# Kernel optimization log

Measured on AMD Instinct MI355X. Metric: run time of the kernel, lower is better.

## Reference

```python
import jax, jax.numpy as jnp
import numpy as np
from jax import lax

DIM = 128; HEADS = 8; SPLIT = 4; MLP = 4
B = 8; H = 64; W = 64
EPS = 1e-5

def conv1x1(x, w, b):
    # x: (b,c,h,w), w: (o,c), b: (o,)
    return jnp.einsum('oc,bchw->bohw', w, x) + b[None, :, None, None]

def dwconv3(x, w, b):
    # depthwise 3x3, w: (C,1,3,3)
    c = x.shape[1]
    y = lax.conv_general_dilated(x, w, window_strides=(1, 1), padding=((1, 1), (1, 1)),
                                 feature_group_count=c,
                                 dimension_numbers=('NCHW', 'OIHW', 'NCHW'))
    return y + b[None, :, None, None]

def groupnorm1(x, g, bta):
    # GroupNorm with 1 group: normalize over (C,H,W) per sample
    mu = x.mean(axis=(1, 2, 3), keepdims=True)
    var = ((x - mu) ** 2).mean(axis=(1, 2, 3), keepdims=True)
    xn = (x - mu) * lax.rsqrt(var + EPS)
    return xn * g[None, :, None, None] + bta[None, :, None, None]

def eca(x, w):
    b, c, h, w_ = x.shape
    y = x.mean(axis=(2, 3))                         # (b,c)
    y = lax.conv_general_dilated(y[:, None, :], w, window_strides=(1,), padding=((2, 2),),
                                 dimension_numbers=('NCH', 'OIH', 'NCH'))  # (b,1,c)
    gate = jax.nn.sigmoid(y[:, 0])[:, :, None, None]
    return x * gate

def esa(x, alpha):
    x_se = x - x.mean(axis=(2, 3), keepdims=True)   # subtract per-channel GAP
    x_max = x_se.max(axis=1, keepdims=True)
    x_min = x_se.min(axis=1, keepdims=True)
    a = alpha[0]
    return x * jax.nn.sigmoid(x_max) * a + x * jax.nn.sigmoid(x_min) * (1.0 - a)

def eaa(q, k, v, h_sp, w_sp, cpe_w, cpe_b):
    b, c, h, w = q.shape
    hd = c // HEADS
    nh, nw = h // h_sp, w // w_sp
    L = h_sp * w_sp
    cpe = dwconv3(v, cpe_w, cpe_b)
    def win(t):
        t = t.reshape(b, c, nh, h_sp, nw, w_sp)
        t = t.transpose(0, 2, 4, 3, 5, 1).reshape(-1, L, HEADS, hd)
        return t.transpose(0, 2, 1, 3)  # (b*nh*nw, heads, L, hd)
    qw, kw, vw = win(q), win(k), win(v)
    attn = jax.nn.softmax(qw @ kw.transpose(0, 1, 3, 2), axis=-1)  # no scale, as in source
    o = attn @ vw                                    # (b*nh*nw, heads, L, hd)
    o = o.transpose(0, 2, 1, 3).reshape(b, nh, nw, h_sp, w_sp, c)
    o = o.transpose(0, 5, 1, 3, 2, 4).reshape(b, c, h, w)
    return o + cpe

def setup_inputs() -> dict:
    key = jax.random.key(0)
    ks = jax.random.split(key, 16)
    d = DIM
    z = lambda *s: jnp.zeros(s, jnp.float32)
    def n(i, shape, s=0.02):
        return jax.random.normal(ks[i], shape, dtype=jnp.float32) * s
    return dict(
        x=jax.random.normal(ks[0], (B, d, H, W), dtype=jnp.float32),
        eca_w=n(1, (1, 1, 5), 0.2),
        esa_alpha=jnp.ones((1,), jnp.float32),
        cpe1_w=n(2, (d, 1, 3, 3), 0.1), cpe1_b=z(d),
        g1=jnp.ones((d,), jnp.float32), b1=z(d),
        actp_w=n(3, (d, d)), actp_b=z(d),
        inp_w=n(4, (d, d)), inp_b=z(d),
        dwc_w=n(5, (d, 1, 3, 3), 0.1), dwc_b=z(d),
        qkv_w=n(6, (5 * d, d)), qkv_b=z(5 * d),
        eaax_w=n(7, (d, 1, 3, 3), 0.1), eaax_b=z(d),
        eaay_w=n(8, (d, 1, 3, 3), 0.1), eaay_b=z(d),
        outp_w=n(9, (d, d)), outp_b=z(d),
        cpe2_w=n(10, (d, 1, 3, 3), 0.1), cpe2_b=z(d),
        g2=jnp.ones((d,), jnp.float32), b2=z(d),
        mlp1_w=n(11, (MLP * d, d)), mlp1_b=z(MLP * d),
        mlp2_w=n(12, (d, MLP * d)), mlp2_b=z(d),
    )

def reference(x, eca_w, esa_alpha, cpe1_w, cpe1_b, g1, b1, actp_w, actp_b, inp_w, inp_b,
              dwc_w, dwc_b, qkv_w, qkv_b, eaax_w, eaax_b, eaay_w, eaay_b, outp_w, outp_b,
              cpe2_w, cpe2_b, g2, b2, mlp1_w, mlp1_b, mlp2_w, mlp2_b):
    b, c, h, w = x.shape
    x = eca(x, eca_w) + esa(x, esa_alpha)
    x = x + dwconv3(x, cpe1_w, cpe1_b)
    shortcut = x
    xn = groupnorm1(x, g1, b1)
    act_res = jax.nn.relu(conv1x1(xn, actp_w, actp_b))
    t = jax.nn.relu(dwconv3(conv1x1(xn, inp_w, inp_b), dwc_w, dwc_b))
    t = conv1x1(t, qkv_w, qkv_b)                     # (b, 5c, h, w)
    t5 = t.reshape(b, c, 5, h, w)                    # channel i::5 == t5[:,:,i]
    q0, k0, v0, q1, k1 = (t5[:, :, i] for i in range(5))
    a = eaa(q0, k0, v0, h, SPLIT, eaax_w, eaax_b) + eaa(q1, k1, v0, SPLIT, w, eaay_w, eaay_b)
    out = conv1x1(a * act_res, outp_w, outp_b) + shortcut
    out = out + dwconv3(out, cpe2_w, cpe2_b)
    mlp = conv1x1(jax.nn.relu(conv1x1(groupnorm1(out, g2, b2), mlp1_w, mlp1_b)), mlp2_w, mlp2_b)
    return mlp + out
```

## Files before the change

kernel.cpp:

```cpp
#include <hip/hip_runtime.h>

#define NPIX 4096
#define CDIM 128
#define BATCH 8
#define EPSN 1e-5f
#define LOG2E 1.44269504088896340736f

typedef __attribute__((ext_vector_type(8))) short short8;
typedef __attribute__((ext_vector_type(4))) float f32x4;
typedef __attribute__((ext_vector_type(16))) float f32x16;

__device__ __forceinline__ float sigmoidf_(float x) { return 1.f / (1.f + __expf(-x)); }

__device__ __forceinline__ unsigned short f2b(float f) {
    unsigned int u = __float_as_uint(f);
    unsigned int r = (u + 0x7FFF + ((u >> 16) & 1)) >> 16;
    return (unsigned short)r;
}
__device__ __forceinline__ float b2f(unsigned short u) {
    return __uint_as_float((unsigned int)u << 16);
}

__device__ __forceinline__ void pl32swap(unsigned int& a, unsigned int& b) {
    asm("v_permlane32_swap_b32 %0, %1" : "+v"(a), "+v"(b));
}

__device__ __forceinline__ int tok2pix(int mode, int wi, int l) {
    return (mode == 0) ? ((l >> 2) * 64 + wi * 4 + (l & 3))
                       : ((wi * 4 + (l >> 6)) * 64 + (l & 63));
}

__global__ __launch_bounds__(256) void convert_w_kernel(const float* __restrict__ qkv_w,
                                                        const float* __restrict__ mlp1_w,
                                                        const float* __restrict__ mlp2_w,
                                                        const float* __restrict__ actp_w,
                                                        const float* __restrict__ inp_w,
                                                        const float* __restrict__ outp_w,
                                                        const float* __restrict__ qkv_b,
                                                        const float* __restrict__ eaax_w,
                                                        const float* __restrict__ eaax_b,
                                                        const float* __restrict__ eaay_w,
                                                        const float* __restrict__ eaay_b,
                                                        const float* __restrict__ cpe1_w,
                                                        const float* __restrict__ dwc_w,
                                                        const float* __restrict__ cpe2_w,
                                                        const float* __restrict__ actp_b,
                                                        const float* __restrict__ inp_b,
                                                        unsigned short* __restrict__ dst,
                                                        float* __restrict__ qb_r,
                                                        float* __restrict__ wsT,
                                                        float* __restrict__ bsum,
                                                        float* __restrict__ cpe1T,
                                                        float* __restrict__ dwcT,
                                                        float* __restrict__ cpe2T,
                                                        float* __restrict__ abi,
                                                        float* __restrict__ gstats) {
    int i = blockIdx.x * 256 + threadIdx.x;
    if (i >= 267776) {
        if (i < 269824) gstats[i - 267776] = 0.f;
        return;
    }
    if (i < 262144) {
        float v;
        if (i < 81920) {
            int o = i >> 7, c = i & 127;
            int g = o >> 7;
            v = qkv_w[(size_t)(5 * (o & 127) + g) * 128 + c];
            if (g == 0 || g == 3) v *= LOG2E;
        } else if (i < 147456) v = mlp1_w[i - 81920];
        else if (i < 212992)   v = mlp2_w[i - 147456];
        else if (i < 229376)   v = actp_w[i - 212992];
        else if (i < 245760)   v = inp_w[i - 229376];
        else                   v = outp_w[i - 245760];
        dst[i] = f2b(v);
    } else {
        int j = i - 262144;
        if (j < 640) {
            int g = j >> 7;
            float v = qkv_b[5 * (j & 127) + g];
            if (g == 0 || g == 3) v *= LOG2E;
            qb_r[j] = v;
        }
        else if (j < 1792) {
            int idx = j - 640; int k = idx >> 7, c = idx & 127;
            wsT[idx] = eaax_w[c * 9 + k] + eaay_w[c * 9 + k];
        } else if (j < 1920) bsum[j - 1792] = eaax_b[j - 1792] + eaay_b[j - 1792];
        else if (j < 3072) {
            int idx = j - 1920; int k = idx >> 7, c = idx & 127;
            cpe1T[idx] = cpe1_w[c * 9 + k];
        } else if (j < 4224) {
            int idx = j - 3072; int k = idx >> 7, c = idx & 127;
            dwcT[idx] = dwc_w[c * 9 + k];
        } else if (j < 5376) {
            int idx = j - 4224; int k = idx >> 7, c = idx & 127;
            cpe2T[idx] = cpe2_w[c * 9 + k];
        } else {
            int idx = j - 5376;
            abi[idx] = (idx < 128) ? actp_b[idx] : inp_b[idx - 128];
        }
    }
}

__global__ __launch_bounds__(256) void mean_bc_kernel(const float* __restrict__ x,
                                                      float* __restrict__ mean) {
    __shared__ float sb[4];
    int bc = blockIdx.x;
    const float* p = x + (size_t)bc * NPIX;
    float s = 0.f;
    for (int i = threadIdx.x; i < NPIX; i += 256) s += p[i];
#pragma unroll
    for (int off = 32; off > 0; off >>= 1) s += __shfl_down(s, off, 64);
    if ((threadIdx.x & 63) == 0) sb[threadIdx.x >> 6] = s;
    __syncthreads();
    if (threadIdx.x == 0) mean[bc] = (sb[0] + sb[1] + sb[2] + sb[3]) * (1.f / (float)NPIX);
}

__global__ __launch_bounds__(256) void esa_tr_kernel(const float* __restrict__ x,
                                                     const float* __restrict__ mean,
                                                     const float* __restrict__ w5,
                                                     const float* __restrict__ alpha_p,
                                                     float* __restrict__ y) {
    __shared__ float tile[128][65];
    __shared__ float smx[4][64], smn[4][64], ssc[64], gat[128];
    int b = blockIdx.y, p0 = blockIdx.x * 64;
    int tx = threadIdx.x, pl = tx & 63, part = tx >> 6;
    const float* xb = x + (size_t)b * CDIM * NPIX;
    const float* mb = mean + b * CDIM;
    for (int c = part; c < CDIM; c += 4)
        tile[c][pl] = xb[(size_t)c * NPIX + p0 + pl];
    __syncthreads();
    float mx = -1e30f, mn = 1e30f;
#pragma unroll
    for (int cc = 0; cc < 32; ++cc) {
        int c = part * 32 + cc;
        float v = tile[c][pl] - mb[c];
        mx = fmaxf(mx, v); mn = fminf(mn, v);
    }
    smx[part][pl] = mx; smn[part][pl] = mn;
    __syncthreads();
    if (tx < 128) {
        float s = 0.f;
#pragma unroll
        for (int k = 0; k < 5; ++k) {
            int cc = tx + k - 2;
            if (cc >= 0 && cc < CDIM) s += w5[k] * mb[cc];
        }
        gat[tx] = sigmoidf_(s);
    }
    if (part == 0) {
        float m1 = fmaxf(fmaxf(smx[0][pl], smx[1][pl]), fmaxf(smx[2][pl], smx[3][pl]));
        float m2 = fminf(fminf(smn[0][pl], smn[1][pl]), fminf(smn[2][pl], smn[3][pl]));
        float a = alpha_p[0];
        ssc[pl] = sigmoidf_(m1) * a + sigmoidf_(m2) * (1.f - a);
    }
    __syncthreads();
    int c2 = tx & 127, pr = tx >> 7;
    float* yb = y + ((size_t)b * NPIX + p0) * CDIM;
    float gv = gat[c2];
    for (int p = pr; p < 64; p += 2)
        yb[(size_t)p * CDIM + c2] = tile[c2][p] * (gv + ssc[p]);
}

__global__ __launch_bounds__(256) void cpe_f32_kernel(const float* __restrict__ in,
                                                      const float* __restrict__ wT,
                                                      const float* __restrict__ bias,
                                                      float* __restrict__ out,
                                                      float* __restrict__ stats) {
    __shared__ float sb[8];
    int b = blockIdx.y, tx = threadIdx.x;
    int cg = tx & 15, pp = tx >> 4;
    int p = blockIdx.x * 16 + pp;
    int xx = p & 63, yy = p >> 6;
    int c0 = cg * 8;
    float acc[8], ctr[8];
#pragma unroll
    for (int j = 0; j < 8; ++j) acc[j] = bias[c0 + j];
#pragma unroll
    for (int dy = -1; dy <= 1; ++dy) {
        int y2 = yy + dy;
        if (y2 < 0 || y2 >= 64) continue;
#pragma unroll
        for (int dx = -1; dx <= 1; ++dx) {
            int x2 = xx + dx;
            if (x2 < 0 || x2 >= 64) continue;
            const float* ip = &in[((size_t)b * NPIX + y2 * 64 + x2) * 128 + c0];
            float4 v0 = *(const float4*)ip;
            float4 v1 = *(const float4*)(ip + 4);
            const float* wr = wT + ((dy + 1) * 3 + dx + 1) * 128 + c0;
            acc[0] += v0.x * wr[0]; acc[1] += v0.y * wr[1];
            acc[2] += v0.z * wr[2]; acc[3] += v0.w * wr[3];
            acc[4] += v1.x * wr[4]; acc[5] += v1.y * wr[5];
            acc[6] += v1.z * wr[6]; acc[7] += v1.w * wr[7];
            if (dy == 0 && dx == 0) {
                ctr[0] = v0.x; ctr[1] = v0.y; ctr[2] = v0.z; ctr[3] = v0.w;
                ctr[4] = v1.x; ctr[5] = v1.y; ctr[6] = v1.z; ctr[7] = v1.w;
            }
        }
    }
    float s = 0.f, s2 = 0.f;
    float r[8];
#pragma unroll
    for (int j = 0; j < 8; ++j) {
        r[j] = ctr[j] + acc[j];
        s += r[j]; s2 += r[j] * r[j];
    }
    float* op = &out[((size_t)b * NPIX + p) * 128 + c0];
    *(float4*)op = make_float4(r[0], r[1], r[2], r[3]);
    *(float4*)(op + 4) = make_float4(r[4], r[5], r[6], r[7]);
#pragma unroll
    for (int off = 32; off > 0; off >>= 1) {
        s += __shfl_down(s, off, 64);
        s2 += __shfl_down(s2, off, 64);
    }
    int wv = tx >> 6;
    if ((tx & 63) == 0) { sb[wv] = s; sb[4 + wv] = s2; }
    __syncthreads();
    if (tx == 0) {
        int slot = (b * 8 + (blockIdx.x & 7)) * 16;
        atomicAdd(&stats[slot], sb[0] + sb[1] + sb[2] + sb[3]);
        atomicAdd(&stats[slot + 1], sb[4] + sb[5] + sb[6] + sb[7]);
    }
}

__global__ __launch_bounds__(256) void dwc_bf16_kernel(const unsigned short* __restrict__ in,
                                                       const float* __restrict__ wT,
                                                       const float* __restrict__ bias,
                                                       unsigned short* __restrict__ out) {
    int b = blockIdx.y, tx = threadIdx.x;
    int cg = tx & 15, pp = tx >> 4;
    int p = blockIdx.x * 16 + pp;
    int xx = p & 63, yy = p >> 6;
    int c0 = cg * 8;
    float acc[8];
#pragma unroll
    for (int j = 0; j < 8; ++j) acc[j] = bias[c0 + j];
#pragma unroll
    for (int dy = -1; dy <= 1; ++dy) {
        int y2 = yy + dy;
        if (y2 < 0 || y2 >= 64) continue;
#pragma unroll
        for (int dx = -1; dx <= 1; ++dx) {
            int x2 = xx + dx;
            if (x2 < 0 || x2 >= 64) continue;
            unsigned short v[8];
            *(uint4*)v = *(const uint4*)&in[((size_t)b * NPIX + y2 * 64 + x2) * 128 + c0];
            const float* wr = wT + ((dy + 1) * 3 + dx + 1) * 128 + c0;
#pragma unroll
            for (int j = 0; j < 8; ++j) acc[j] += b2f(v[j]) * wr[j];
        }
    }
    unsigned short o[8];
#pragma unroll
    for (int j = 0; j < 8; ++j) o[j] = f2b(fmaxf(acc[j], 0.f));
    *(uint4*)&out[((size_t)b * NPIX + p) * 128 + c0] = *(uint4*)o;
}

__global__ __launch_bounds__(256) void conv_mfma_kernel(const unsigned short* __restrict__ in_t,
                                                        const float* __restrict__ in_f32,
                                                        const float* __restrict__ gst,
                                                        const float* __restrict__ gg,
                                                        const float* __restrict__ gbta,
                                                        const unsigned short* __restrict__ w,
                                                        const float* __restrict__ bias,
                                                        const float* __restrict__ res,
                                                        float* __restrict__ out,
                                                        unsigned short* __restrict__ out_t,
                                                        unsigned short* __restrict__ out_t2,
                                                        int Cin, int Cout, int relu, int nchw) {
    __shared__ __align__(16) unsigned short A_s[128][136];
    __shared__ __align__(16) unsigned short B_s[64][136];
    int b = blockIdx.z, p0 = blockIdx.x * 64, o0 = blockIdx.y * 128;
    int tx = threadIdx.x;
    int wave = tx >> 6, lane = tx & 63;
    int wm = wave & 1, wn = wave >> 1;
    int quad = lane >> 4, l16 = lane & 15;

    float mu = 0.f, rr = 1.f;
    if (in_f32) {
        float su = 0.f, sq = 0.f;
#pragma unroll
        for (int sl = 0; sl < 8; ++sl) {
            su += gst[(b * 8 + sl) * 16];
            sq += gst[(b * 8 + sl) * 16 + 1];
        }
        const float n = 1.f / (float)(CDIM * NPIX);
        mu = su * n;
        float var = sq * n - mu * mu;
        rr = rsqrtf(var + EPSN);
    }

    f32x4 acc[4][2];
#pragma unroll
    for (int mt = 0; mt < 4; ++mt) {
#pragma unroll
        for (int r = 0; r < 4; ++r) {
            float bv = bias[o0 + wm * 64 + mt * 16 + quad * 4 + r];
#pragma unroll
            for (int nt = 0; nt < 2; ++nt) acc[mt][nt][r] = bv;
        }
    }

    for (int k0 = 0; k0 < Cin; k0 += 128) {
#pragma unroll
        for (int j = 0; j < 8; ++j) {
            int idx = tx + 256 * j;
            int row = idx >> 4, c16 = idx & 15;
            *(uint4*)&A_s[row][c16 * 8] =
                *(const uint4*)&w[(size_t)(o0 + row) * Cin + k0 + c16 * 8];
        }
        if (in_f32) {
#pragma unroll
            for (int j = 0; j < 4; ++j) {
                int idx = tx + 256 * j;
                int row = idx >> 4, c16 = idx & 15;
                int ch = c16 * 8;
                const float* ip = &in_f32[((size_t)b * NPIX + p0 + row) * 128 + ch];
                float4 v0 = *(const float4*)ip;
                float4 v1 = *(const float4*)(ip + 4);
                unsigned short o[8];
                o[0] = f2b((v0.x - mu) * rr * gg[ch + 0] + gbta[ch + 0]);
                o[1] = f2b((v0.y - mu) * rr * gg[ch + 1] + gbta[ch + 1]);
                o[2] = f2b((v0.z - mu) * rr * gg[ch + 2] + gbta[ch + 2]);
                o[3] = f2b((v0.w - mu) * rr * gg[ch + 3] + gbta[ch + 3]);
                o[4] = f2b((v1.x - mu) * rr * gg[ch + 4] + gbta[ch + 4]);
                o[5] = f2b((v1.y - mu) * rr * gg[ch + 5] + gbta[ch + 5]);
                o[6] = f2b((v1.z - mu) * rr * gg[ch + 6] + gbta[ch + 6]);
                o[7] = f2b((v1.w - mu) * rr * gg[ch + 7] + gbta[ch + 7]);
                *(uint4*)&B_s[row][c16 * 8] = *(uint4*)o;
            }
        } else {
#pragma unroll
            for (int j = 0; j < 4; ++j) {
                int idx = tx + 256 * j;
                int row = idx >> 4, c16 = idx & 15;
                *(uint4*)&B_s[row][c16 * 8] =
                    *(const uint4*)&in_t[((size_t)b * NPIX + p0 + row) * Cin + k0 + c16 * 8];
            }
        }
        __syncthreads();
#pragma unroll
        for (int ks = 0; ks < 128; ks += 32) {
            short8 af[4], bf[2];
#pragma unroll
            for (int mt = 0; mt < 4; ++mt)
                af[mt] = *(const short8*)&A_s[wm * 64 + mt * 16 + l16][ks + quad * 8];
#pragma unroll
            for (int nt = 0; nt < 2; ++nt)
                bf[nt] = *(const short8*)&B_s[wn * 32 + nt * 16 + l16][ks + quad * 8];
#pragma unroll
            for (int mt = 0; mt < 4; ++mt)
#pragma unroll
                for (int nt = 0; nt < 2; ++nt)
                    acc[mt][nt] = __builtin_amdgcn_mfma_f32_16x16x32_bf16(
                        af[mt], bf[nt], acc[mt][nt], 0, 0, 0);
        }
        __syncthreads();
    }

    int dorelu = (relu == 1) || (relu == 2 && blockIdx.y == 0);
    if (out_t) {
#pragma unroll
        for (int mt = 0; mt < 4; ++mt) {
#pragma unroll
            for (int nt = 0; nt < 2; ++nt) {
                int p = p0 + wn * 32 + nt * 16 + l16;
                int ob = o0 + wm * 64 + mt * 16 + quad * 4;
                unsigned short* dbuf = out_t;
                int oc = ob;
                if (out_t2 && o0 >= 128) { dbuf = out_t2; oc = ob - 128; }
                ushort4 u;
                float v0 = acc[mt][nt][0], v1 = acc[mt][nt][1];
                float v2 = acc[mt][nt][2], v3 = acc[mt][nt][3];
                if (dorelu) { v0 = fmaxf(v0, 0.f); v1 = fmaxf(v1, 0.f);
                              v2 = fmaxf(v2, 0.f); v3 = fmaxf(v3, 0.f); }
                u.x = f2b(v0); u.y = f2b(v1); u.z = f2b(v2); u.w = f2b(v3);
                *(ushort4*)&dbuf[((size_t)b * NPIX + p) * Cout + oc] = u;
            }
        }
    } else if (!nchw) {
#pragma unroll
        for (int mt = 0; mt < 4; ++mt) {
#pragma unroll
            for (int nt = 0; nt < 2; ++nt) {
                int p = p0 + wn * 32 + nt * 16 + l16;
                int ob = o0 + wm * 64 + mt * 16 + quad * 4;
                size_t ix = ((size_t)b * NPIX + p) * Cout + ob;
                float4 v = make_float4(acc[mt][nt][0], acc[mt][nt][1],
                                       acc[mt][nt][2], acc[mt][nt][3]);
                if (dorelu) { v.x = fmaxf(v.x, 0.f); v.y = fmaxf(v.y, 0.f);
                              v.z = fmaxf(v.z, 0.f); v.w = fmaxf(v.w, 0.f); }
                if (res) {
                    float4 rv = *(const float4*)&res[ix];
                    v.x += rv.x; v.y += rv.y; v.z += rv.z; v.w += rv.w;
                }
                *(float4*)&out[ix] = v;
            }
        }
    } else {
        float* outb = out + (size_t)b * Cout * NPIX;
#pragma unroll
        for (int mt = 0; mt < 4; ++mt) {
#pragma unroll
            for (int nt = 0; nt < 2; ++nt) {
                int p = p0 + wn * 32 + nt * 16 + l16;
                int ob = o0 + wm * 64 + mt * 16 + quad * 4;
                float4 rv = make_float4(0.f, 0.f, 0.f, 0.f);
                if (res) rv = *(const float4*)&res[((size_t)b * NPIX + p) * 128 + ob];
#pragma unroll
                for (int r = 0; r < 4; ++r) {
                    float v = acc[mt][nt][r];
                    if (dorelu) v = fmaxf(v, 0.f);
                    v += (r == 0 ? rv.x : r == 1 ? rv.y : r == 2 ? rv.z : rv.w);
                    outb[(size_t)(ob + r) * NPIX + p] = v;
                }
            }
        }
    }
}

__global__ __launch_bounds__(256) void attn_dual_kernel(const unsigned short* __restrict__ t_t,
                                                        float* __restrict__ a0,
                                                        float* __restrict__ a1) {
    __shared__ __align__(16) unsigned short Vt[32][264];
    __shared__ __align__(16) unsigned short Kt[256][24];
    int wi = blockIdx.x, head = blockIdx.y;
    int z = blockIdx.z;
    int b = z >> 1, which = z & 1;
    int qoff = which ? 384 : 0;
    int koff = which ? 512 : 128;
    int mode = which;
    float* a_out = which ? a1 : a0;
    int tx = threadIdx.x;
    int wave = tx >> 6, l = tx & 63;
    int l32 = l & 31, half = l >> 5;
    const size_t base = (size_t)b * NPIX;
    const int hc = head * 16;

    {
        int p = tok2pix(mode, wi, tx);
        const unsigned short* vp = &t_t[(base + p) * 640 + 256 + hc];
        const unsigned short* kp = &t_t[(base + p) * 640 + koff + hc];
        unsigned short tmp[16];
        *(uint4*)&tmp[0] = *(const uint4*)vp;
        *(uint4*)&tmp[8] = *(const uint4*)(vp + 8);
        uint4 k0 = *(const uint4*)kp;
        uint4 k1 = *(const uint4*)(kp + 8);
        *(uint4*)&Kt[tx][0] = k0;
        *(uint4*)&Kt[tx][8] = k1;
#pragma unroll
        for (int d = 0; d < 16; ++d) Vt[d][tx] = tmp[d];
        Vt[16][tx] = (unsigned short)0x3F80;
#pragma unroll
        for (int d = 17; d < 32; ++d) Vt[d][tx] = 0;
    }
    __syncthreads();

    f32x16 zzero;
#pragma unroll
    for (int r = 0; r < 16; ++r) zzero[r] = 0.f;

    const unsigned short* qb = t_t + base * 640 + hc + half * 8 + qoff;

    int qp0 = tok2pix(mode, wi, (0 * 4 + wave) * 32 + l32);
    int qp1 = tok2pix(mode, wi, (1 * 4 + wave) * 32 + l32);
    short8 qf0 = *(const short8*)&qb[(size_t)qp0 * 640];
    short8 qf1 = *(const short8*)&qb[(size_t)qp1 * 640];
    f32x16 oa0 = zzero, oa1 = zzero;

#pragma unroll
    for (int nt = 0; nt < 8; ++nt) {
        short8 kf = *(const short8*)&Kt[nt * 32 + l32][half * 8];
        short8 vf0 = *(const short8*)&Vt[l32][nt * 32 + half * 8];
        short8 vf1 = *(const short8*)&Vt[l32][nt * 32 + 16 + half * 8];
#pragma unroll
        for (int qi = 0; qi < 2; ++qi) {
            short8 qf = (qi == 0) ? qf0 : qf1;
            f32x16 s = __builtin_amdgcn_mfma_f32_32x32x16_bf16(kf, qf, zzero, 0, 0, 0);
            unsigned int pk[8];
#pragma unroll
            for (int i = 0; i < 8; ++i) {
                float e0 = __builtin_amdgcn_exp2f(s[2 * i]);
                float e1 = __builtin_amdgcn_exp2f(s[2 * i + 1]);
                pk[i] = __builtin_amdgcn_perm(__float_as_uint(e1), __float_as_uint(e0),
                                              0x07060302u);
            }
            pl32swap(pk[0], pk[2]);
            pl32swap(pk[1], pk[3]);
            pl32swap(pk[4], pk[6]);
            pl32swap(pk[5], pk[7]);
            unsigned int u0[4] = {pk[0], pk[1], pk[2], pk[3]};
            unsigned int u1[4] = {pk[4], pk[5], pk[6], pk[7]};
            if (qi == 0) {
                oa0 = __builtin_amdgcn_mfma_f32_32x32x16_bf16(vf0, *(short8*)u0, oa0, 0, 0, 0);
                oa0 = __builtin_amdgcn_mfma_f32_32x32x16_bf16(vf1, *(short8*)u1, oa0, 0, 0, 0);
            } else {
                oa1 = __builtin_amdgcn_mfma_f32_32x32x16_bf16(vf0, *(short8*)u0, oa1, 0, 0, 0);
                oa1 = __builtin_amdgcn_mfma_f32_32x32x16_bf16(vf1, *(short8*)u1, oa1, 0, 0, 0);
            }
        }
    }

#pragma unroll
    for (int qi = 0; qi < 2; ++qi) {
        f32x16 oc = (qi == 0) ? oa0 : oa1;
        int qp = (qi == 0) ? qp0 : qp1;
        float rs = oc[8];
        rs += __shfl_xor(rs, 32, 64);
        float rinv = 1.f / rs;
        float* dst = a_out + (base + qp) * 128 + hc + 4 * half;
        float4 s0 = make_float4(oc[0] * rinv, oc[1] * rinv,
                                oc[2] * rinv, oc[3] * rinv);
        float4 s1 = make_float4(oc[4] * rinv, oc[5] * rinv,
                                oc[6] * rinv, oc[7] * rinv);
        *(float4*)dst = s0;
        *(float4*)(dst + 8) = s1;
    }
}

__global__ __launch_bounds__(256) void mul3_cpe_kernel(const float* __restrict__ a0,
                                                       const float* __restrict__ a1,
                                                       const unsigned short* __restrict__ act,
                                                       const unsigned short* __restrict__ t_t,
                                                       const float* __restrict__ wT,
                                                       const float* __restrict__ bsum,
                                                       unsigned short* __restrict__ dst) {
    int b = blockIdx.y;
    int tx = threadIdx.x;
    int cg = tx & 15, pp = tx >> 4;
    int p = blockIdx.x * 16 + pp;
    int xx = p & 63, yy = p >> 6;
    int c0 = cg * 8;
    float acc[8];
#pragma unroll
    for (int j = 0; j < 8; ++j) acc[j] = bsum[c0 + j];
#pragma unroll
    for (int dy = -1; dy <= 1; ++dy) {
        int y2 = yy + dy;
        if (y2 < 0 || y2 >= 64) continue;
#pragma unroll
        for (int dx = -1; dx <= 1; ++dx) {
            int x2 = xx + dx;
            if (x2 < 0 || x2 >= 64) continue;
            int pn = y2 * 64 + x2;
            unsigned short v[8];
            *(uint4*)v = *(const uint4*)&t_t[((size_t)b * NPIX + pn) * 640 + 256 + c0];
            const float* wr = wT + ((dy + 1) * 3 + dx + 1) * 128 + c0;
#pragma unroll
            for (int j = 0; j < 8; ++j) acc[j] += b2f(v[j]) * wr[j];
        }
    }
    size_t base = ((size_t)b * NPIX + p) * 128 + c0;
    float4 x0 = *(const float4*)&a0[base];
    float4 x1 = *(const float4*)&a0[base + 4];
    float4 y0 = *(const float4*)&a1[base];
    float4 y1 = *(const float4*)&a1[base + 4];
    unsigned short t[8];
    *(uint4*)t = *(const uint4*)&act[base];
    unsigned short r[8];
    r[0] = f2b((x0.x + y0.x + acc[0]) * b2f(t[0]));
    r[1] = f2b((x0.y + y0.y + acc[1]) * b2f(t[1]));
    r[2] = f2b((x0.z + y0.z + acc[2]) * b2f(t[2]));
    r[3] = f2b((x0.w + y0.w + acc[3]) * b2f(t[3]));
    r[4] = f2b((x1.x + y1.x + acc[4]) * b2f(t[4]));
    r[5] = f2b((x1.y + y1.y + acc[5]) * b2f(t[5]));
    r[6] = f2b((x1.z + y1.z + acc[6]) * b2f(t[6]));
    r[7] = f2b((x1.w + y1.w + acc[7]) * b2f(t[7]));
    *(uint4*)&dst[base] = *(uint4*)r;
}

extern "C" void kernel_launch(void* const* d_in, const int* in_sizes, int n_in,
                              void* d_out, int out_size, void* d_ws, size_t ws_size,
                              hipStream_t stream) {
    const float* x       = (const float*)d_in[0];
    const float* eca_w   = (const float*)d_in[1];
    const float* esa_al  = (const float*)d_in[2];
    const float* cpe1_w  = (const float*)d_in[3];  const float* cpe1_b = (const float*)d_in[4];
    const float* g1      = (const float*)d_in[5];  const float* b1     = (const float*)d_in[6];
    const float* actp_w  = (const float*)d_in[7];  const float* actp_b = (const float*)d_in[8];
    const float* inp_w   = (const float*)d_in[9];  const float* inp_b  = (const float*)d_in[10];
    const float* dwc_w   = (const float*)d_in[11]; const float* dwc_b  = (const float*)d_in[12];
    const float* qkv_w   = (const float*)d_in[13]; const float* qkv_b  = (const float*)d_in[14];
    const float* eaax_w  = (const float*)d_in[15]; const float* eaax_b = (const float*)d_in[16];
    const float* eaay_w  = (const float*)d_in[17]; const float* eaay_b = (const float*)d_in[18];
    const float* outp_w  = (const float*)d_in[19]; const float* outp_b = (const float*)d_in[20];
    const float* cpe2_w  = (const float*)d_in[21]; const float* cpe2_b = (const float*)d_in[22];
    const float* g2      = (const float*)d_in[23]; const float* b2     = (const float*)d_in[24];
    const float* mlp1_w  = (const float*)d_in[25]; const float* mlp1_b = (const float*)d_in[26];
    const float* mlp2_w  = (const float*)d_in[27]; const float* mlp2_b = (const float*)d_in[28];

    float* ws = (float*)d_ws;
    unsigned short* U = (unsigned short*)d_ws;
    const size_t E = (size_t)BATCH * CDIM * NPIX;

    float* y_nhwc  = ws;
    float* a0      = ws;
    float* sc_nhwc = ws + E;
    unsigned short* act_t = U + 5 * E;
    unsigned short* it_t  = U + 6 * E;
    unsigned short* tin_t = U + 7 * E;
    float* a1      = ws + 4 * E;
    unsigned short* t_t   = U + 10 * E;
    unsigned short* m_t   = U + 15 * E;
    float* out_nhwc = ws + 8 * E;
    float* out2    = ws + 2 * E;
    unsigned short* hid_t = U + 10 * E;
    unsigned short* wpool = U + 20 * E;
    unsigned short* wq  = wpool;
    unsigned short* wm1 = wpool + 81920;
    unsigned short* wm2 = wpool + 147456;
    unsigned short* wai = wpool + 212992;
    unsigned short* wo  = wpool + 245760;
    float* fb     = ws + 10 * E + 131072;
    float* meanb  = fb;
    float* gstats = fb + 2048;
    float* qb_r   = fb + 4096;
    float* wsT    = fb + 4736;
    float* bsum   = fb + 5888;
    float* cpe1T  = fb + 6016;
    float* dwcT   = fb + 7168;
    float* cpe2T  = fb + 8320;
    float* abi    = fb + 9472;

    convert_w_kernel<<<1054, 256, 0, stream>>>(qkv_w, mlp1_w, mlp2_w, actp_w, inp_w, outp_w,
                                               qkv_b, eaax_w, eaax_b, eaay_w, eaay_b,
                                               cpe1_w, dwc_w, cpe2_w, actp_b, inp_b,
                                               wpool, qb_r, wsT, bsum, cpe1T, dwcT, cpe2T, abi,
                                               gstats);

    mean_bc_kernel<<<BATCH * CDIM, 256, 0, stream>>>(x, meanb);
    esa_tr_kernel<<<dim3(64, BATCH), 256, 0, stream>>>(x, meanb, eca_w, esa_al, y_nhwc);
    cpe_f32_kernel<<<dim3(256, BATCH), 256, 0, stream>>>(y_nhwc, cpe1T, cpe1_b, sc_nhwc, gstats);
    conv_mfma_kernel<<<dim3(64, 2, BATCH), 256, 0, stream>>>(nullptr, sc_nhwc, gstats, g1, b1,
                                                             wai, abi, nullptr, nullptr,
                                                             act_t, it_t, 128, 128, 2, 0);
    dwc_bf16_kernel<<<dim3(256, BATCH), 256, 0, stream>>>(it_t, dwcT, dwc_b, tin_t);
    conv_mfma_kernel<<<dim3(64, 5, BATCH), 256, 0, stream>>>(tin_t, nullptr, nullptr, nullptr,
                                                             nullptr, wq, qb_r, nullptr, nullptr,
                                                             t_t, nullptr, 128, 640, 0, 0);
    attn_dual_kernel<<<dim3(16, 8, 2 * BATCH), 256, 0, stream>>>(t_t, a0, a1);
    mul3_cpe_kernel<<<dim3(256, BATCH), 256, 0, stream>>>(a0, a1, act_t, t_t, wsT, bsum, m_t);
    conv_mfma_kernel<<<dim3(64, 1, BATCH), 256, 0, stream>>>(m_t, nullptr, nullptr, nullptr,
                                                             nullptr, wo, outp_b, sc_nhwc,
                                                             out_nhwc, nullptr, nullptr,
                                                             128, 128, 0, 0);
    cpe_f32_kernel<<<dim3(256, BATCH), 256, 0, stream>>>(out_nhwc, cpe2T, cpe2_b, out2,
                                                         gstats + 1024);
    conv_mfma_kernel<<<dim3(64, 4, BATCH), 256, 0, stream>>>(nullptr, out2, gstats + 1024, g2, b2,
                                                             wm1, mlp1_b, nullptr, nullptr,
                                                             hid_t, nullptr, 128, 512, 1, 0);
    conv_mfma_kernel<<<dim3(64, 1, BATCH), 256, 0, stream>>>(hid_t, nullptr, nullptr, nullptr,
                                                             nullptr, wm2, mlp2_b, out2,
                                                             (float*)d_out, nullptr, nullptr,
                                                             512, 128, 0, 1);
}
```

Baseline: 292.3 us.

## Store attention outputs as bf16 and shrink V shared-memory tile

The attention kernel now writes its per-window outputs a0/a1 as bf16 instead of fp32, and the following multiply/CPE kernel reads them as bf16. This halves the intermediate traffic between the two kernels. The V tile in shared memory drops from 32 rows to 18, with rows above 17 clamped to a zero row, which cuts LDS footprint and initialisation stores. The trade-off is extra rounding of the attention outputs before they are summed.

```diff
diff --git a/kernel.cpp b/kernel.cpp
--- a/kernel.cpp
+++ b/kernel.cpp
@@ -419,9 +419,9 @@
 }
 
 __global__ __launch_bounds__(256) void attn_dual_kernel(const unsigned short* __restrict__ t_t,
-                                                        float* __restrict__ a0,
-                                                        float* __restrict__ a1) {
-    __shared__ __align__(16) unsigned short Vt[32][264];
+                                                        unsigned short* __restrict__ a0,
+                                                        unsigned short* __restrict__ a1) {
+    __shared__ __align__(16) unsigned short Vt[18][264];
     __shared__ __align__(16) unsigned short Kt[256][24];
     int wi = blockIdx.x, head = blockIdx.y;
     int z = blockIdx.z;
@@ -429,7 +429,7 @@
     int qoff = which ? 384 : 0;
     int koff = which ? 512 : 128;
     int mode = which;
-    float* a_out = which ? a1 : a0;
+    unsigned short* a_out = which ? a1 : a0;
     int tx = threadIdx.x;
     int wave = tx >> 6, l = tx & 63;
     int l32 = l & 31, half = l >> 5;
@@ -450,14 +450,16 @@
 #pragma unroll
         for (int d = 0; d < 16; ++d) Vt[d][tx] = tmp[d];
         Vt[16][tx] = (unsigned short)0x3F80;
-#pragma unroll
-        for (int d = 17; d < 32; ++d) Vt[d][tx] = 0;
+        Vt[17][tx] = 0;
     }
     __syncthreads();
 
     f32x16 zzero;
 #pragma unroll
     for (int r = 0; r < 16; ++r) zzero[r] = 0.f;
+
+    int vrow = (l32 < 17) ? l32 : 17;
+    const unsigned short* vbase = &Vt[vrow][0];
 
     const unsigned short* qb = t_t + base * 640 + hc + half * 8 + qoff;
 
@@ -470,8 +472,8 @@
 #pragma unroll
     for (int nt = 0; nt < 8; ++nt) {
         short8 kf = *(const short8*)&Kt[nt * 32 + l32][half * 8];
-        short8 vf0 = *(const short8*)&Vt[l32][nt * 32 + half * 8];
-        short8 vf1 = *(const short8*)&Vt[l32][nt * 32 + 16 + half * 8];
+        short8 vf0 = *(const short8*)&vbase[nt * 32 + half * 8];
+        short8 vf1 = *(const short8*)&vbase[nt * 32 + 16 + half * 8];
 #pragma unroll
         for (int qi = 0; qi < 2; ++qi) {
             short8 qf = (qi == 0) ? qf0 : qf1;
@@ -507,18 +509,19 @@
         float rs = oc[8];
         rs += __shfl_xor(rs, 32, 64);
         float rinv = 1.f / rs;
-        float* dst = a_out + (base + qp) * 128 + hc + 4 * half;
-        float4 s0 = make_float4(oc[0] * rinv, oc[1] * rinv,
-                                oc[2] * rinv, oc[3] * rinv);
-        float4 s1 = make_float4(oc[4] * rinv, oc[5] * rinv,
-                                oc[6] * rinv, oc[7] * rinv);
-        *(float4*)dst = s0;
-        *(float4*)(dst + 8) = s1;
-    }
-}
-
-__global__ __launch_bounds__(256) void mul3_cpe_kernel(const float* __restrict__ a0,
-                                                       const float* __restrict__ a1,
+        unsigned short* dst = a_out + (base + qp) * 128 + hc + 4 * half;
+        ushort4 s0, s1;
+        s0.x = f2b(oc[0] * rinv); s0.y = f2b(oc[1] * rinv);
+        s0.z = f2b(oc[2] * rinv); s0.w = f2b(oc[3] * rinv);
+        s1.x = f2b(oc[4] * rinv); s1.y = f2b(oc[5] * rinv);
+        s1.z = f2b(oc[6] * rinv); s1.w = f2b(oc[7] * rinv);
+        *(ushort4*)dst = s0;
+        *(ushort4*)(dst + 8) = s1;
+    }
+}
+
+__global__ __launch_bounds__(256) void mul3_cpe_kernel(const unsigned short* __restrict__ a0,
+                                                       const unsigned short* __restrict__ a1,
                                                        const unsigned short* __restrict__ act,
                                                        const unsigned short* __restrict__ t_t,
                                                        const float* __restrict__ wT,
@@ -550,21 +553,14 @@
         }
     }
     size_t base = ((size_t)b * NPIX + p) * 128 + c0;
-    float4 x0 = *(const float4*)&a0[base];
-    float4 x1 = *(const float4*)&a0[base + 4];
-    float4 y0 = *(const float4*)&a1[base];
-    float4 y1 = *(const float4*)&a1[base + 4];
-    unsigned short t[8];
-    *(uint4*)t = *(const uint4*)&act[base];
+    unsigned short xa[8], ya[8], t[8];
+    *(uint4*)xa = *(const uint4*)&a0[base];
+    *(uint4*)ya = *(const uint4*)&a1[base];
+    *(uint4*)t  = *(const uint4*)&act[base];
     unsigned short r[8];
-    r[0] = f2b((x0.x + y0.x + acc[0]) * b2f(t[0]));
-    r[1] = f2b((x0.y + y0.y + acc[1]) * b2f(t[1]));
-    r[2] = f2b((x0.z + y0.z + acc[2]) * b2f(t[2]));
-    r[3] = f2b((x0.w + y0.w + acc[3]) * b2f(t[3]));
-    r[4] = f2b((x1.x + y1.x + acc[4]) * b2f(t[4]));
-    r[5] = f2b((x1.y + y1.y + acc[5]) * b2f(t[5]));
-    r[6] = f2b((x1.z + y1.z + acc[6]) * b2f(t[6]));
-    r[7] = f2b((x1.w + y1.w + acc[7]) * b2f(t[7]));
+#pragma unroll
+    for (int j = 0; j < 8; ++j)
+        r[j] = f2b((b2f(xa[j]) + b2f(ya[j]) + acc[j]) * b2f(t[j]));
     *(uint4*)&dst[base] = *(uint4*)r;
 }
 
@@ -593,12 +589,12 @@
     const size_t E = (size_t)BATCH * CDIM * NPIX;
 
     float* y_nhwc  = ws;
-    float* a0      = ws;
+    unsigned short* a0b = U;
     float* sc_nhwc = ws + E;
     unsigned short* act_t = U + 5 * E;
     unsigned short* it_t  = U + 6 * E;
     unsigned short* tin_t = U + 7 * E;
-    float* a1      = ws + 4 * E;
+    unsigned short* a1b   = U + 8 * E;
     unsigned short* t_t   = U + 10 * E;
     unsigned short* m_t   = U + 15 * E;
     float* out_nhwc = ws + 8 * E;
@@ -637,8 +633,8 @@
     conv_mfma_kernel<<<dim3(64, 5, BATCH), 256, 0, stream>>>(tin_t, nullptr, nullptr, nullptr,
                                                              nullptr, wq, qb_r, nullptr, nullptr,
                                                              t_t, nullptr, 128, 640, 0, 0);
-    attn_dual_kernel<<<dim3(16, 8, 2 * BATCH), 256, 0, stream>>>(t_t, a0, a1);
-    mul3_cpe_kernel<<<dim3(256, BATCH), 256, 0, stream>>>(a0, a1, act_t, t_t, wsT, bsum, m_t);
+    attn_dual_kernel<<<dim3(16, 8, 2 * BATCH), 256, 0, stream>>>(t_t, a0b, a1b);
+    mul3_cpe_kernel<<<dim3(256, BATCH), 256, 0, stream>>>(a0b, a1b, act_t, t_t, wsT, bsum, m_t);
     conv_mfma_kernel<<<dim3(64, 1, BATCH), 256, 0, stream>>>(m_t, nullptr, nullptr, nullptr,
                                                              nullptr, wo, outp_b, sc_nhwc,
                                                              out_nhwc, nullptr, nullptr,
```

Result: no change. 290.6 us (-0.6%).
